# Kernel optimization log

Hardware: AMD Instinct MI355X
Metric: run time of the kernel (lower is better)

## Reference

```python
import jax, jax.numpy as jnp
import numpy as np

NUM_EXPERTS = 8
TOP_K = 2


def setup_inputs() -> dict:
    key = jax.random.key(0)
    ks = jax.random.split(key, 6)
    B, S, D, H, E = 4, 1024, 1024, 2048, NUM_EXPERTS
    x = jax.random.normal(ks[0], (B, S, D), dtype=jnp.float32)
    Wg = jax.random.normal(ks[1], (D, E), dtype=jnp.float32) * 0.02
    W1 = jax.random.normal(ks[2], (E, D, H), dtype=jnp.float32) * 0.02
    b1 = jax.random.normal(ks[3], (E, H), dtype=jnp.float32) * 0.02
    W2 = jax.random.normal(ks[4], (E, H, D), dtype=jnp.float32) * 0.02
    b2 = jax.random.normal(ks[5], (E, D), dtype=jnp.float32) * 0.02
    return {"x": x, "Wg": Wg, "W1": W1, "b1": b1, "W2": W2, "b2": b2}


def reference(x, Wg, W1, b1, W2, b2):
    B, S, D = x.shape
    E, _, H = W1.shape
    OUT = W2.shape[2]
    xm = x.reshape(-1, D)                      # [N, D], N = B*S
    # --- top-k gating (ProbabilitySamplerTopk): softmax over experts, take top-k ---
    logits = xm @ Wg                           # [N, E]
    probs = jax.nn.softmax(logits, axis=-1)
    topk_p, topk_i = jax.lax.top_k(probs, TOP_K)   # [N, K]
    # --- sort dispatched (token, expert) pairs by expert id (stable) ---
    flat_e = topk_i.reshape(-1)                # [N*K]
    flat_p = topk_p.reshape(-1)                # [N*K]
    order = jnp.argsort(flat_e)                # stable sort -> grouped by expert
    tok_idx = order // TOP_K                   # source token index (trunc-div by topK)
    e_sorted = flat_e[order]                   # [N*K]
    p_sorted = flat_p[order]                   # [N*K]
    xs = xm[tok_idx]                           # [N*K, D] expert-sorted inputs
    # --- grouped-GEMM experts: masked per-expert dense GEMM (E is small & fixed) ---
    y = jnp.zeros((xs.shape[0], OUT), dtype=xs.dtype)
    for e in range(E):
        h = jax.nn.relu(xs @ W1[e] + b1[e])    # [N*K, H]
        ye = h @ W2[e] + b2[e]                 # [N*K, OUT]
        m = (e_sorted == e)[:, None].astype(xs.dtype)
        y = y + m * ye
    # --- combine: multiply by gates, scatter-add back to token slots ---
    y = y * p_sorted[:, None]
    out = jnp.zeros((B * S, OUT), dtype=y.dtype).at[tok_idx].add(y)
    return out.reshape(B, S, OUT)
```

## Files before the change

### kernel.cpp

```cpp
#include <hip/hip_runtime.h>
#include <hip/hip_bf16.h>
#include <stdint.h>

typedef __bf16 bf16;
typedef __bf16 bf16x8 __attribute__((ext_vector_type(8)));
typedef __bf16 bf16x4 __attribute__((ext_vector_type(4)));
typedef float f32x4 __attribute__((ext_vector_type(4)));

#define N_TOK 4096
#define DDIM 1024
#define HDIM 2048
#define NPAIR 8192
#define MT128 71
#define MT256 39

__device__ __forceinline__ void gload16(const void* g, void* l) {
  __builtin_amdgcn_global_load_lds(
      (const __attribute__((address_space(1))) unsigned int*)g,
      (__attribute__((address_space(3))) unsigned int*)l, 16, 0, 0);
}

__global__ void transpose_cvt_kernel(const float* __restrict__ in, bf16* __restrict__ out,
                                     int R, int C) {
  __shared__ float tile[32][33];
  const float* ip = in + (size_t)blockIdx.z * R * C;
  bf16* op = out + (size_t)blockIdx.z * R * C;
  int r0 = blockIdx.y * 32, c0 = blockIdx.x * 32;
  int tr = threadIdx.x >> 3;
  int tc = (threadIdx.x & 7) * 4;
  float4 v = *(const float4*)(ip + (size_t)(r0 + tr) * C + c0 + tc);
  tile[tr][tc] = v.x; tile[tr][tc + 1] = v.y; tile[tr][tc + 2] = v.z; tile[tr][tc + 3] = v.w;
  __syncthreads();
  bf16x4 o = {(bf16)tile[tc + 0][tr], (bf16)tile[tc + 1][tr],
              (bf16)tile[tc + 2][tr], (bf16)tile[tc + 3][tr]};
  *(bf16x4*)(op + (size_t)(c0 + tr) * R + r0 + tc) = o;
}

__global__ void gate_kernel(const float* __restrict__ x, const float* __restrict__ Wg,
                            int2* __restrict__ ge, float2* __restrict__ gp,
                            bf16* __restrict__ xb) {
  int t = blockIdx.x * 4 + (threadIdx.x >> 6);
  int lane = threadIdx.x & 63;
  const float* xr = x + (size_t)t * DDIM;
  bf16* xbr = xb + (size_t)t * DDIM;
  float a[8];
#pragma unroll
  for (int e = 0; e < 8; e++) a[e] = 0.f;
#pragma unroll
  for (int it = 0; it < 4; it++) {
    int d0 = it * 256 + lane * 4;
    float4 xv = *(const float4*)(xr + d0);
    bf16x4 o = {(bf16)xv.x, (bf16)xv.y, (bf16)xv.z, (bf16)xv.w};
    *(bf16x4*)(xbr + d0) = o;
    float xs[4] = {xv.x, xv.y, xv.z, xv.w};
#pragma unroll
    for (int dd = 0; dd < 4; dd++) {
      float4 w0 = *(const float4*)(Wg + (size_t)(d0 + dd) * 8);
      float4 w1 = *(const float4*)(Wg + (size_t)(d0 + dd) * 8 + 4);
      a[0] += xs[dd] * w0.x; a[1] += xs[dd] * w0.y; a[2] += xs[dd] * w0.z; a[3] += xs[dd] * w0.w;
      a[4] += xs[dd] * w1.x; a[5] += xs[dd] * w1.y; a[6] += xs[dd] * w1.z; a[7] += xs[dd] * w1.w;
    }
  }
#pragma unroll
  for (int off = 32; off >= 1; off >>= 1) {
#pragma unroll
    for (int e = 0; e < 8; e++) a[e] += __shfl_xor(a[e], off);
  }
  if (lane == 0) {
    float m = a[0];
#pragma unroll
    for (int e = 1; e < 8; e++) m = fmaxf(m, a[e]);
    float p[8]; float s = 0.f;
#pragma unroll
    for (int e = 0; e < 8; e++) { p[e] = expf(a[e] - m); s += p[e]; }
    float inv = 1.f / s;
    int i0 = 0; float v0 = a[0];
#pragma unroll
    for (int e = 1; e < 8; e++) if (a[e] > v0) { v0 = a[e]; i0 = e; }
    int i1 = -1; float v1 = -1e30f;
#pragma unroll
    for (int e = 0; e < 8; e++) if (e != i0 && a[e] > v1) { v1 = a[e]; i1 = e; }
    ge[t] = make_int2(i0, i1);
    gp[t] = make_float2(p[i0] * inv, p[i1] * inv);
  }
}

__global__ void sort_kernel(const int2* __restrict__ ge, const float2* __restrict__ gp,
                            int* __restrict__ tok, float* __restrict__ ps,
                            int* __restrict__ meta) {
  __shared__ int hist[8], runn[8], wc[16][8], wb[16][8], baseS[9];
  int tid = threadIdx.x;
  int lane = tid & 63, wv = tid >> 6;
  if (tid < 8) hist[tid] = 0;
  __syncthreads();
  for (int i = tid; i < NPAIR; i += 1024) {
    int2 g = ge[i >> 1];
    int e = (i & 1) ? g.y : g.x;
    atomicAdd(&hist[e], 1);
  }
  __syncthreads();
  if (tid == 0) {
    int b = 0, ts1 = 0, ts2 = 0;
    for (int e = 0; e < 8; e++) {
      baseS[e] = b; meta[e] = b;
      meta[9 + e] = ts1;  ts1 += (hist[e] + 127) / 128;
      meta[18 + e] = ts2; ts2 += (hist[e] + 255) / 256;
      b += hist[e];
    }
    baseS[8] = b; meta[8] = b; meta[17] = ts1; meta[26] = ts2;
  }
  __syncthreads();
  if (tid < 8) runn[tid] = baseS[tid];
  __syncthreads();
  for (int c = 0; c < 8; c++) {
    int i = c * 1024 + tid;
    int2 g = ge[i >> 1];
    int e = (i & 1) ? g.y : g.x;
    int rank = 0;
#pragma unroll
    for (int ee = 0; ee < 8; ee++) {
      unsigned long long b = __ballot(e == ee);
      if (e == ee) rank = __popcll(b & ((1ull << lane) - 1ull));
      if (lane == 0) wc[wv][ee] = __popcll(b);
    }
    __syncthreads();
    if (tid < 8) {
      int s = runn[tid];
      for (int w = 0; w < 16; w++) { wb[w][tid] = s; s += wc[w][tid]; }
      runn[tid] = s;
    }
    __syncthreads();
    int pos = wb[wv][e] + rank;
    tok[pos] = i >> 1;
    float2 p2 = gp[i >> 1];
    ps[pos] = (i & 1) ? p2.y : p2.x;
    __syncthreads();
  }
}

__global__ void zero_kernel(float4* __restrict__ p) {
  p[blockIdx.x * 256 + threadIdx.x] = make_float4(0.f, 0.f, 0.f, 0.f);
}

template <int KDIM, int NPE, bool FIRST, int BMT, int THREADS, int NT, int MAPOFF>
__global__ __launch_bounds__(THREADS, (THREADS == 256) ? 3 : 4)
void moe_gemm_kernel(const bf16* __restrict__ A, const bf16* __restrict__ Bt,
                     const float* __restrict__ bias, const int* __restrict__ tok,
                     const float* __restrict__ ps, const int* __restrict__ meta,
                     bf16* __restrict__ hout, float* __restrict__ outp) {
  constexpr int AR = BMT * 4 / THREADS;
  constexpr int BR = 128 * 4 / THREADS;
  constexpr int SLOT = (BMT + 128) * 32;
  __shared__ bf16 lds[3][SLOT];

  int MTa = meta[MAPOFF + 8];
  int xcd = blockIdx.x & 7;
  int idx = blockIdx.x >> 3;
  int mLo = (MTa * xcd) >> 3;
  int mHi = (MTa * (xcd + 1)) >> 3;
  int cnt = mHi - mLo;
  if (idx >= cnt * NT) return;
  int tileN = idx / cnt;
  int tileM = mLo + idx - tileN * cnt;

  int e = 0;
#pragma unroll
  for (int k = 1; k < 8; k++) if (tileM >= meta[MAPOFF + k]) e = k;
  int row0 = meta[e] + (tileM - meta[MAPOFF + e]) * BMT;
  int segEnd = meta[e + 1];
  int n0 = tileN * 128;

  int t = threadIdx.x;
  const bf16* aSrc[AR];
  const bf16* bSrc[BR];
  {
    int swz = ((t & 3) ^ ((t >> 3) & 3)) * 8;
#pragma unroll
    for (int r = 0; r < AR; r++) {
      int row = r * (THREADS / 4) + (t >> 2);
      int gRow = row0 + row; if (gRow > NPAIR - 1) gRow = NPAIR - 1;
      int arow = FIRST ? tok[gRow] : gRow;
      aSrc[r] = A + (size_t)arow * KDIM + swz;
    }
#pragma unroll
    for (int r = 0; r < BR; r++) {
      int row = r * (THREADS / 4) + (t >> 2);
      bSrc[r] = Bt + ((size_t)e * NPE + n0 + row) * KDIM + swz;
    }
  }

  int lane = t & 63, wv = t >> 6;
  int wm = wv >> 1, wn = wv & 1;
  int l15 = lane & 15, l4 = lane >> 4;
  int aOff[4], bOff[4];
#pragma unroll
  for (int m = 0; m < 4; m++) {
    int row = wm * 64 + m * 16 + l15;
    aOff[m] = row * 32 + ((l4 ^ ((row >> 1) & 3)) * 8);
  }
#pragma unroll
  for (int n = 0; n < 4; n++) {
    int row = wn * 64 + n * 16 + l15;
    bOff[n] = BMT * 32 + row * 32 + ((l4 ^ ((row >> 1) & 3)) * 8);
  }

  f32x4 acc[4][4];
#pragma unroll
  for (int m = 0; m < 4; m++)
#pragma unroll
    for (int n = 0; n < 4; n++)
#pragma unroll
      for (int j = 0; j < 4; j++) acc[m][n][j] = 0.f;

  auto STAGE = [&](int kt, int slot) {
    bf16* sb = &lds[slot][0];
    int ko = kt * 32;
#pragma unroll
    for (int r = 0; r < AR; r++) gload16(aSrc[r] + ko, sb + (r * THREADS + t) * 8);
#pragma unroll
    for (int r = 0; r < BR; r++) gload16(bSrc[r] + ko, sb + BMT * 32 + (r * THREADS + t) * 8);
  };

  constexpr int nk = KDIM / 32;
  STAGE(0, 0);
  STAGE(1, 1);
  for (int kt = 0; kt < nk; kt++) {
    if (kt == nk - 1) asm volatile("s_waitcnt vmcnt(0)\n\ts_barrier" ::: "memory");
    else if constexpr (AR + BR == 4) asm volatile("s_waitcnt vmcnt(4)\n\ts_barrier" ::: "memory");
    else                             asm volatile("s_waitcnt vmcnt(3)\n\ts_barrier" ::: "memory");
    if (kt + 2 < nk) STAGE(kt + 2, (kt + 2) % 3);
    __builtin_amdgcn_sched_barrier(0);
    const bf16* sb = &lds[kt % 3][0];
    bf16x8 af[4], bfr[4];
#pragma unroll
    for (int m = 0; m < 4; m++) af[m] = *(const bf16x8*)(sb + aOff[m]);
#pragma unroll
    for (int n = 0; n < 4; n++) bfr[n] = *(const bf16x8*)(sb + bOff[n]);
    __builtin_amdgcn_s_setprio(1);
#pragma unroll
    for (int m = 0; m < 4; m++)
#pragma unroll
      for (int n = 0; n < 4; n++)
        acc[m][n] = __builtin_amdgcn_mfma_f32_16x16x32_bf16(af[m], bfr[n], acc[m][n], 0, 0, 0);
    __builtin_amdgcn_s_setprio(0);
  }

  int colb = n0 + wn * 64 + l15;
  int rowb = wm * 64 + l4 * 4;
  float bia[4];
#pragma unroll
  for (int n = 0; n < 4; n++) bia[n] = bias[(size_t)e * NPE + colb + n * 16];
#pragma unroll
  for (int m = 0; m < 4; m++) {
#pragma unroll
    for (int j = 0; j < 4; j++) {
      int gRow = row0 + rowb + m * 16 + j;
      if (gRow < segEnd) {
        if (FIRST) {
#pragma unroll
          for (int n = 0; n < 4; n++) {
            float v = acc[m][n][j] + bia[n];
            v = fmaxf(v, 0.f);
            hout[(size_t)gRow * NPE + colb + n * 16] = (bf16)v;
          }
        } else {
          float pscale = ps[gRow];
          float* orow = outp + (size_t)tok[gRow] * DDIM;
#pragma unroll
          for (int n = 0; n < 4; n++) {
            float v = (acc[m][n][j] + bia[n]) * pscale;
            atomicAdd(orow + colb + n * 16, v);
          }
        }
      }
    }
  }
}

extern "C" void kernel_launch(void* const* d_in, const int* in_sizes, int n_in,
                              void* d_out, int out_size, void* d_ws, size_t ws_size,
                              hipStream_t stream) {
  (void)in_sizes; (void)n_in; (void)ws_size;
  const float* x  = (const float*)d_in[0];
  const float* Wg = (const float*)d_in[1];
  const float* W1 = (const float*)d_in[2];
  const float* b1 = (const float*)d_in[3];
  const float* W2 = (const float*)d_in[4];
  const float* b2 = (const float*)d_in[5];
  float* out = (float*)d_out;

  char* ws = (char*)d_ws;
  bf16*  xb   = (bf16*)(ws);
  bf16*  W1T  = (bf16*)(ws + (8ull  << 20));
  bf16*  W2T  = (bf16*)(ws + (40ull << 20));
  bf16*  hbuf = (bf16*)(ws + (72ull << 20));
  char*  ext  = ws + (104ull << 20);
  int2*   ge      = (int2*)(ext);
  float2* gp      = (float2*)(ext + (64u  << 10));
  int*    tok     = (int*)(ext + (128u << 10));
  float*  psarr   = (float*)(ext + (160u << 10));
  int*    meta    = (int*)(ext + (224u << 10));

  transpose_cvt_kernel<<<dim3(64, 32, 8), 256, 0, stream>>>(W1, W1T, 1024, 2048);
  transpose_cvt_kernel<<<dim3(32, 64, 8), 256, 0, stream>>>(W2, W2T, 2048, 1024);
  gate_kernel<<<1024, 256, 0, stream>>>(x, Wg, ge, gp, xb);
  sort_kernel<<<1, 1024, 0, stream>>>(ge, gp, tok, psarr, meta);
  zero_kernel<<<out_size / 1024, 256, 0, stream>>>((float4*)out);
  moe_gemm_kernel<1024, 2048, true, 128, 256, 16, 9><<<dim3(1152), 256, 0, stream>>>(
      xb, W1T, b1, tok, psarr, meta, hbuf, nullptr);
  moe_gemm_kernel<2048, 1024, false, 256, 512, 8, 18><<<dim3(320), 512, 0, stream>>>(
      hbuf, W2T, b2, tok, psarr, meta, nullptr, out);
}
```

Measured before the change: 201.4 us.

## Use 128-row tiles for second GEMM and fold output zeroing into gate kernel

```diff
diff --git a/kernel.cpp b/kernel.cpp
--- a/kernel.cpp
+++ b/kernel.cpp
@@ -11,8 +11,6 @@
 #define DDIM 1024
 #define HDIM 2048
 #define NPAIR 8192
-#define MT128 71
-#define MT256 39
 
 __device__ __forceinline__ void gload16(const void* g, void* l) {
   __builtin_amdgcn_global_load_lds(
@@ -38,8 +36,15 @@
 
 __global__ void gate_kernel(const float* __restrict__ x, const float* __restrict__ Wg,
                             int2* __restrict__ ge, float2* __restrict__ gp,
-                            bf16* __restrict__ xb) {
-  int t = blockIdx.x * 4 + (threadIdx.x >> 6);
+                            bf16* __restrict__ xb, float* __restrict__ outp) {
+  int t0 = blockIdx.x * 4;
+  {
+    float4 z = make_float4(0.f, 0.f, 0.f, 0.f);
+    float4* ob = (float4*)(outp + (size_t)t0 * DDIM);
+#pragma unroll
+    for (int r = 0; r < 4; r++) ob[r * 256 + threadIdx.x] = z;
+  }
+  int t = t0 + (threadIdx.x >> 6);
   int lane = threadIdx.x & 63;
   const float* xr = x + (size_t)t * DDIM;
   bf16* xbr = xb + (size_t)t * DDIM;
@@ -100,14 +105,13 @@
   }
   __syncthreads();
   if (tid == 0) {
-    int b = 0, ts1 = 0, ts2 = 0;
+    int b = 0, ts1 = 0;
     for (int e = 0; e < 8; e++) {
       baseS[e] = b; meta[e] = b;
       meta[9 + e] = ts1;  ts1 += (hist[e] + 127) / 128;
-      meta[18 + e] = ts2; ts2 += (hist[e] + 255) / 256;
       b += hist[e];
     }
-    baseS[8] = b; meta[8] = b; meta[17] = ts1; meta[26] = ts2;
+    baseS[8] = b; meta[8] = b; meta[17] = ts1;
   }
   __syncthreads();
   if (tid < 8) runn[tid] = baseS[tid];
@@ -138,22 +142,15 @@
   }
 }
 
-__global__ void zero_kernel(float4* __restrict__ p) {
-  p[blockIdx.x * 256 + threadIdx.x] = make_float4(0.f, 0.f, 0.f, 0.f);
-}
-
-template <int KDIM, int NPE, bool FIRST, int BMT, int THREADS, int NT, int MAPOFF>
-__global__ __launch_bounds__(THREADS, (THREADS == 256) ? 3 : 4)
+template <int KDIM, int NPE, bool FIRST, int NT>
+__global__ __launch_bounds__(256, 3)
 void moe_gemm_kernel(const bf16* __restrict__ A, const bf16* __restrict__ Bt,
                      const float* __restrict__ bias, const int* __restrict__ tok,
                      const float* __restrict__ ps, const int* __restrict__ meta,
                      bf16* __restrict__ hout, float* __restrict__ outp) {
-  constexpr int AR = BMT * 4 / THREADS;
-  constexpr int BR = 128 * 4 / THREADS;
-  constexpr int SLOT = (BMT + 128) * 32;
-  __shared__ bf16 lds[3][SLOT];
-
-  int MTa = meta[MAPOFF + 8];
+  __shared__ bf16 lds[3][8192];
+
+  int MTa = meta[17];
   int xcd = blockIdx.x & 7;
   int idx = blockIdx.x >> 3;
   int mLo = (MTa * xcd) >> 3;
@@ -165,26 +162,22 @@
 
   int e = 0;
 #pragma unroll
-  for (int k = 1; k < 8; k++) if (tileM >= meta[MAPOFF + k]) e = k;
-  int row0 = meta[e] + (tileM - meta[MAPOFF + e]) * BMT;
+  for (int k = 1; k < 8; k++) if (tileM >= meta[9 + k]) e = k;
+  int row0 = meta[e] + (tileM - meta[9 + e]) * 128;
   int segEnd = meta[e + 1];
   int n0 = tileN * 128;
 
   int t = threadIdx.x;
-  const bf16* aSrc[AR];
-  const bf16* bSrc[BR];
+  const bf16* aSrc[2];
+  const bf16* bSrc[2];
   {
     int swz = ((t & 3) ^ ((t >> 3) & 3)) * 8;
 #pragma unroll
-    for (int r = 0; r < AR; r++) {
-      int row = r * (THREADS / 4) + (t >> 2);
+    for (int r = 0; r < 2; r++) {
+      int row = r * 64 + (t >> 2);
       int gRow = row0 + row; if (gRow > NPAIR - 1) gRow = NPAIR - 1;
       int arow = FIRST ? tok[gRow] : gRow;
       aSrc[r] = A + (size_t)arow * KDIM + swz;
-    }
-#pragma unroll
-    for (int r = 0; r < BR; r++) {
-      int row = r * (THREADS / 4) + (t >> 2);
       bSrc[r] = Bt + ((size_t)e * NPE + n0 + row) * KDIM + swz;
     }
   }
@@ -201,7 +194,7 @@
 #pragma unroll
   for (int n = 0; n < 4; n++) {
     int row = wn * 64 + n * 16 + l15;
-    bOff[n] = BMT * 32 + row * 32 + ((l4 ^ ((row >> 1) & 3)) * 8);
+    bOff[n] = 4096 + row * 32 + ((l4 ^ ((row >> 1) & 3)) * 8);
   }
 
   f32x4 acc[4][4];
@@ -215,10 +208,10 @@
   auto STAGE = [&](int kt, int slot) {
     bf16* sb = &lds[slot][0];
     int ko = kt * 32;
-#pragma unroll
-    for (int r = 0; r < AR; r++) gload16(aSrc[r] + ko, sb + (r * THREADS + t) * 8);
-#pragma unroll
-    for (int r = 0; r < BR; r++) gload16(bSrc[r] + ko, sb + BMT * 32 + (r * THREADS + t) * 8);
+    gload16(aSrc[0] + ko, sb + t * 8);
+    gload16(aSrc[1] + ko, sb + 2048 + t * 8);
+    gload16(bSrc[0] + ko, sb + 4096 + t * 8);
+    gload16(bSrc[1] + ko, sb + 6144 + t * 8);
   };
 
   constexpr int nk = KDIM / 32;
@@ -226,8 +219,7 @@
   STAGE(1, 1);
   for (int kt = 0; kt < nk; kt++) {
     if (kt == nk - 1) asm volatile("s_waitcnt vmcnt(0)\n\ts_barrier" ::: "memory");
-    else if constexpr (AR + BR == 4) asm volatile("s_waitcnt vmcnt(4)\n\ts_barrier" ::: "memory");
-    else                             asm volatile("s_waitcnt vmcnt(3)\n\ts_barrier" ::: "memory");
+    else              asm volatile("s_waitcnt vmcnt(4)\n\ts_barrier" ::: "memory");
     if (kt + 2 < nk) STAGE(kt + 2, (kt + 2) % 3);
     __builtin_amdgcn_sched_barrier(0);
     const bf16* sb = &lds[kt % 3][0];
@@ -280,7 +272,7 @@
 extern "C" void kernel_launch(void* const* d_in, const int* in_sizes, int n_in,
                               void* d_out, int out_size, void* d_ws, size_t ws_size,
                               hipStream_t stream) {
-  (void)in_sizes; (void)n_in; (void)ws_size;
+  (void)in_sizes; (void)n_in; (void)out_size; (void)ws_size;
   const float* x  = (const float*)d_in[0];
   const float* Wg = (const float*)d_in[1];
   const float* W1 = (const float*)d_in[2];
@@ -303,11 +295,10 @@
 
   transpose_cvt_kernel<<<dim3(64, 32, 8), 256, 0, stream>>>(W1, W1T, 1024, 2048);
   transpose_cvt_kernel<<<dim3(32, 64, 8), 256, 0, stream>>>(W2, W2T, 2048, 1024);
-  gate_kernel<<<1024, 256, 0, stream>>>(x, Wg, ge, gp, xb);
+  gate_kernel<<<1024, 256, 0, stream>>>(x, Wg, ge, gp, xb, out);
   sort_kernel<<<1, 1024, 0, stream>>>(ge, gp, tok, psarr, meta);
-  zero_kernel<<<out_size / 1024, 256, 0, stream>>>((float4*)out);
-  moe_gemm_kernel<1024, 2048, true, 128, 256, 16, 9><<<dim3(1152), 256, 0, stream>>>(
+  moe_gemm_kernel<1024, 2048, true, 16><<<dim3(1152), 256, 0, stream>>>(
       xb, W1T, b1, tok, psarr, meta, hbuf, nullptr);
-  moe_gemm_kernel<2048, 1024, false, 256, 512, 8, 18><<<dim3(320), 512, 0, stream>>>(
+  moe_gemm_kernel<2048, 1024, false, 8><<<dim3(576), 256, 0, stream>>>(
       hbuf, W2T, b2, tok, psarr, meta, nullptr, out);
 }
```

Measured after the change: 197.8 us. About the same (-1.8%).
